# Performance work log

Measured on AMD Instinct MI355X. Metric: run time of the kernel, lower is better.

The kernel has to match this reference:

```python
import jax, jax.numpy as jnp
import numpy as np

NUM_HEADS = 4  # nn.MultiheadAttention(num_heads=4)


def setup_inputs() -> dict:
    key = jax.random.key(0)
    ks = jax.random.split(key, 9)
    E, D, B, S = 16, 128, 8, 512
    H2 = D // 2
    s = 0.05
    return {
        "lstm_features": jax.random.normal(ks[0], (B, S, D), dtype=jnp.float32),
        "Wqkv": jax.random.normal(ks[1], (E, 3 * D, D), dtype=jnp.float32) * s,
        "bqkv": jax.random.normal(ks[2], (E, 3 * D), dtype=jnp.float32) * s,
        "Wo": jax.random.normal(ks[3], (E, D, D), dtype=jnp.float32) * s,
        "bo": jax.random.normal(ks[4], (E, D), dtype=jnp.float32) * s,
        "W1": jax.random.normal(ks[5], (E, H2, D), dtype=jnp.float32) * s,
        "b1": jax.random.normal(ks[6], (E, H2), dtype=jnp.float32) * s,
        "W2": jax.random.normal(ks[7], (E, 1, H2), dtype=jnp.float32) * s,
        "b2": jax.random.normal(ks[8], (E, 1), dtype=jnp.float32) * s,
    }


def reference(lstm_features, Wqkv, bqkv, Wo, bo, W1, b1, W2, b2):
    # lstm_features: [B, S, D]; params stacked over E=num_events.
    B, S, D = lstm_features.shape
    E = Wqkv.shape[0]
    H = NUM_HEADS
    Dh = D // H

    # Grouped in-projection for all events at once: [E, B, S, 3D]
    qkv = jnp.einsum("bsd,ekd->ebsk", lstm_features, Wqkv) + bqkv[:, None, None, :]
    q, k, v = jnp.split(qkv, 3, axis=-1)  # each [E, B, S, D]

    def heads(t):  # [E,B,S,D] -> [E,B,H,S,Dh]
        return t.reshape(E, B, S, H, Dh).transpose(0, 1, 3, 2, 4)

    q, k, v = heads(q), heads(k), heads(v)

    scale = 1.0 / jnp.sqrt(jnp.asarray(Dh, dtype=lstm_features.dtype))
    scores = jnp.einsum("ebhqd,ebhkd->ebhqk", q, k) * scale  # [E,B,H,S,S]
    attn = jax.nn.softmax(scores, axis=-1)
    ctx = jnp.einsum("ebhqk,ebhkd->ebhqd", attn, v)  # [E,B,H,S,Dh]
    ctx = ctx.transpose(0, 1, 3, 2, 4).reshape(E, B, S, D)

    attended = jnp.einsum("ebsd,eod->ebso", ctx, Wo) + bo[:, None, None, :]

    # Per-event MLP head: D -> D//2 -> 1 (dropout is identity in eval)
    h = jax.nn.relu(jnp.einsum("ebsd,ehd->ebsh", attended, W1) + b1[:, None, None, :])
    logits = jnp.einsum("ebsh,eoh->ebso", h, W2) + b2[:, None, None, :]  # [E,B,S,1]
    logits = logits[..., 0]  # [E,B,S]

    # torch.stack(..., dim=2) -> [B, S, E]
    return logits.transpose(1, 2, 0)
```

## Files before the change

### kernel.cpp

```cpp
#include <hip/hip_runtime.h>
#include <hip/hip_bf16.h>


#define E_ 16
#define B_ 8
#define S_ 512
#define D_ 128
#define H_ 4
#define DH_ 32
#define H2_ 64
#define M_ (B_ * S_)
#define QK_SCALE_L2E 0.25503472437616588f

typedef __attribute__((ext_vector_type(4))) short bf16x4;
typedef __attribute__((ext_vector_type(8))) short bf16x8;
typedef __attribute__((ext_vector_type(4))) float f32x4;

__device__ __forceinline__ short f2bf(float f) {
    unsigned u = __builtin_bit_cast(unsigned, f);
    u += 0x7fffu + ((u >> 16) & 1u);
    return (short)(u >> 16);
}

__device__ __forceinline__ unsigned pk2(float lo, float hi) {
    __hip_bfloat162 t = __float22bfloat162_rn(make_float2(lo, hi));
    unsigned r;
    __builtin_memcpy(&r, &t, sizeof(r));
    return r;
}

__device__ __forceinline__ bf16x8 cat8(bf16x4 lo, bf16x4 hi) {
    return __builtin_shufflevector(lo, hi, 0, 1, 2, 3, 4, 5, 6, 7);
}

__global__ __launch_bounds__(256) void convert_kernel(
    const float* __restrict__ x, const float* __restrict__ w,
    const float* __restrict__ wo, const float* __restrict__ w1,
    short* __restrict__ xbf, short* __restrict__ wbf,
    short* __restrict__ wobf, short* __restrict__ w1bf)
{
    const int XN  = (M_ * D_) / 8;
    const int WN  = (E_ * 3 * D_ * D_) / 8;
    const int WON = (E_ * D_ * D_) / 8;
    const int W1N = (E_ * H2_ * D_) / 8;
    int idx = blockIdx.x * 256 + threadIdx.x;
    const float* src; short* dst; int off;
    if (idx < XN)                        { src = x;  dst = xbf;  off = idx; }
    else if (idx < XN + WN)              { src = w;  dst = wbf;  off = idx - XN; }
    else if (idx < XN + WN + WON)        { src = wo; dst = wobf; off = idx - XN - WN; }
    else if (idx < XN + WN + WON + W1N)  { src = w1; dst = w1bf; off = idx - XN - WN - WON; }
    else return;
    float4 v0 = *(const float4*)&src[(size_t)off * 8];
    float4 v1 = *(const float4*)&src[(size_t)off * 8 + 4];
    bf16x8 o;
    o[0] = f2bf(v0.x); o[1] = f2bf(v0.y); o[2] = f2bf(v0.z); o[3] = f2bf(v0.w);
    o[4] = f2bf(v1.x); o[5] = f2bf(v1.y); o[6] = f2bf(v1.z); o[7] = f2bf(v1.w);
    *(bf16x8*)&dst[(size_t)off * 8] = o;
}

__global__ __launch_bounds__(256) void qkv_mfma_kernel(
    const short* __restrict__ xbf,
    const short* __restrict__ wbf,
    const float* __restrict__ bqkv,
    short* __restrict__ q, short* __restrict__ k, short* __restrict__ v)
{
    __shared__ __align__(16) char lds[2 * 64 * 136 * 2];
    short (*xs)[136] = (short(*)[136])lds;
    short (*ws)[136] = (short(*)[136])(lds + 64 * 136 * 2);

    const int ct = blockIdx.x;
    const int rt = blockIdx.y;
    const int e  = blockIdx.z;
    const int tid = threadIdx.x;
    const int w    = tid >> 6;
    const int lane = tid & 63;
    const int l15  = lane & 15;
    const int g    = lane >> 4;

    #pragma unroll
    for (int p = 0; p < 4; ++p) {
        int idx = tid + p * 256;
        int row = idx >> 4, c8 = (idx & 15) * 8;
        *(bf16x8*)&xs[row][c8] =
            *(const bf16x8*)&xbf[(size_t)(rt * 64 + row) * 128 + c8];
        *(bf16x8*)&ws[row][c8] =
            *(const bf16x8*)&wbf[((size_t)e * 384 + ct * 64 + row) * 128 + c8];
    }
    __syncthreads();

    const int n0 = (w & 1) * 32;
    const int m0 = (w >> 1) * 32;
    f32x4 acc00 = {0.f,0.f,0.f,0.f}, acc01 = {0.f,0.f,0.f,0.f};
    f32x4 acc10 = {0.f,0.f,0.f,0.f}, acc11 = {0.f,0.f,0.f,0.f};

    #pragma unroll
    for (int kk = 0; kk < 128; kk += 32) {
        bf16x8 A0 = cat8(*(const bf16x4*)&ws[n0      + l15][kk + 4 * g],
                         *(const bf16x4*)&ws[n0      + l15][kk + 16 + 4 * g]);
        bf16x8 A1 = cat8(*(const bf16x4*)&ws[n0 + 16 + l15][kk + 4 * g],
                         *(const bf16x4*)&ws[n0 + 16 + l15][kk + 16 + 4 * g]);
        bf16x8 B0 = cat8(*(const bf16x4*)&xs[m0      + l15][kk + 4 * g],
                         *(const bf16x4*)&xs[m0      + l15][kk + 16 + 4 * g]);
        bf16x8 B1 = cat8(*(const bf16x4*)&xs[m0 + 16 + l15][kk + 4 * g],
                         *(const bf16x4*)&xs[m0 + 16 + l15][kk + 16 + 4 * g]);
        acc00 = __builtin_amdgcn_mfma_f32_16x16x32_bf16(A0, B0, acc00, 0, 0, 0);
        acc01 = __builtin_amdgcn_mfma_f32_16x16x32_bf16(A0, B1, acc01, 0, 0, 0);
        acc10 = __builtin_amdgcn_mfma_f32_16x16x32_bf16(A1, B0, acc10, 0, 0, 0);
        acc11 = __builtin_amdgcn_mfma_f32_16x16x32_bf16(A1, B1, acc11, 0, 0, 0);
    }

    if (ct < 4) {
        short* dst = (ct < 2) ? q : k;
        const float scale = (ct < 2) ? QK_SCALE_L2E : 1.0f;
        #define STORE_QK(ACC, NS, MS) {                                          \
            const int jb = ct * 64 + n0 + (NS) * 16 + 4 * g;                     \
            const int d  = jb & 127;                                             \
            const int h  = d >> 5, dh = d & 31;                                  \
            const float b0 = bqkv[e * 384 + jb + 0];                             \
            const float b1 = bqkv[e * 384 + jb + 1];                             \
            const float b2 = bqkv[e * 384 + jb + 2];                             \
            const float b3 = bqkv[e * 384 + jb + 3];                             \
            const int m  = rt * 64 + m0 + (MS) * 16 + l15;                       \
            const int bb = m >> 9, s = m & 511;                                  \
            bf16x4 o;                                                            \
            o[0] = f2bf((ACC[0] + b0) * scale);                                  \
            o[1] = f2bf((ACC[1] + b1) * scale);                                  \
            o[2] = f2bf((ACC[2] + b2) * scale);                                  \
            o[3] = f2bf((ACC[3] + b3) * scale);                                  \
            *(bf16x4*)&dst[((((size_t)e * B_ + bb) * H_ + h) * S_ + s) * DH_ + dh] = o; \
        }
        STORE_QK(acc00, 0, 0); STORE_QK(acc01, 0, 1);
        STORE_QK(acc10, 1, 0); STORE_QK(acc11, 1, 1);
        #undef STORE_QK
    } else {
        __syncthreads();
        float (*rp)[68] = (float(*)[68])lds;
        #define RP(ACC, NS, MS) {                                                \
            const int jl = n0 + (NS) * 16 + 4 * g;                               \
            const int ml = m0 + (MS) * 16 + l15;                                 \
            rp[jl + 0][ml] = ACC[0]; rp[jl + 1][ml] = ACC[1];                    \
            rp[jl + 2][ml] = ACC[2]; rp[jl + 3][ml] = ACC[3];                    \
        }
        RP(acc00, 0, 0); RP(acc01, 0, 1); RP(acc10, 1, 0); RP(acc11, 1, 1);
        #undef RP
        __syncthreads();
        const int bb = (rt * 64) >> 9;
        const int sb = (rt * 64) & 511;
        #pragma unroll
        for (int p = 0; p < 2; ++p) {
            int task = tid + p * 256;
            int jl = task >> 3, sc = (task & 7) * 8;
            const int col = ct * 64 + jl;
            const int d = col & 127, h = d >> 5, dh = d & 31;
            const float bias = bqkv[e * 384 + col];
            bf16x8 o;
            #pragma unroll
            for (int j = 0; j < 8; ++j) o[j] = f2bf(rp[jl][sc + j] + bias);
            *(bf16x8*)&v[((((size_t)e * B_ + bb) * H_ + h) * DH_ + dh) * S_ + sb + sc] = o;
        }
    }
}

__global__ __launch_bounds__(512) void attn_kernel(
    const short* __restrict__ q, const short* __restrict__ k,
    const short* __restrict__ vt, short* __restrict__ ctxbf)
{
    __shared__ alignas(16) short Ks[128][40];
    __shared__ alignas(16) short VTs[32][520];

    const int qh  = blockIdx.x;
    const int bh  = blockIdx.y;
    const int e   = blockIdx.z;
    const int tid = threadIdx.x;
    const int w    = tid >> 6;
    const int lane = tid & 63;
    const int l15  = lane & 15;
    const int g    = lane >> 4;

    const size_t base = ((size_t)e * 32 + bh) * (S_ * DH_);
    const short* qg = q  + base;
    const short* kg = k  + base;
    const short* vg = vt + base;

    {
        int d = tid >> 4, c0 = (tid & 15) * 32;
        const uint4* src = (const uint4*)(vg + (size_t)d * S_ + c0);
        uint4* dst = (uint4*)((char*)&VTs[0][0] + (size_t)d * 1040 + c0 * 2);
        dst[0] = src[0]; dst[1] = src[1]; dst[2] = src[2]; dst[3] = src[3];
    }
    {
        int row = tid >> 2, ch = (tid & 3) * 8;
        *(uint4*)((char*)&Ks[0][0] + (size_t)row * 80 + ch * 2) =
            *(const uint4*)(kg + (size_t)row * DH_ + ch);
    }
    bf16x8 bq[2];
    #pragma unroll
    for (int qf = 0; qf < 2; ++qf) {
        const short* qp = qg + (size_t)(qh * 256 + w * 32 + qf * 16 + l15) * DH_;
        bq[qf] = cat8(*(const bf16x4*)(qp + 4 * g),
                      *(const bf16x4*)(qp + 16 + 4 * g));
    }
    __syncthreads();

    f32x4 acc0[2] = {}, acc1[2] = {};
    float lsum[2] = {0.f, 0.f};

    for (int quarter = 0; quarter < 4; ++quarter) {
        for (int kt = 0; kt < 4; ++kt) {
            bf16x8 ka[2];
            #pragma unroll
            for (int tt = 0; tt < 2; ++tt) {
                const int row_l = (kt * 2 + tt) * 16 + l15;
                const char* kp = (const char*)&Ks[0][0] + (size_t)row_l * 80 + g * 8;
                ka[tt] = cat8(*(const bf16x4*)kp, *(const bf16x4*)(kp + 32));
            }
            const int keyb = quarter * 128 + kt * 32;
            const char* vp = (const char*)&VTs[0][0] + (size_t)l15 * 1040 + (keyb + 4 * g) * 2;
            bf16x8 va0 = cat8(*(const bf16x4*)vp, *(const bf16x4*)(vp + 32));
            const char* vp1 = vp + 16 * 1040;
            bf16x8 va1 = cat8(*(const bf16x4*)vp1, *(const bf16x4*)(vp1 + 32));

            #pragma unroll
            for (int qf = 0; qf < 2; ++qf) {
                f32x4 z = {0.f, 0.f, 0.f, 0.f};
                f32x4 s0 = __builtin_amdgcn_mfma_f32_16x16x32_bf16(ka[0], bq[qf], z, 0, 0, 0);
                f32x4 s1 = __builtin_amdgcn_mfma_f32_16x16x32_bf16(ka[1], bq[qf], z, 0, 0, 0);
                float p0 = __builtin_amdgcn_exp2f(s0[0]);
                float p1 = __builtin_amdgcn_exp2f(s0[1]);
                float p2 = __builtin_amdgcn_exp2f(s0[2]);
                float p3 = __builtin_amdgcn_exp2f(s0[3]);
                float p4 = __builtin_amdgcn_exp2f(s1[0]);
                float p5 = __builtin_amdgcn_exp2f(s1[1]);
                float p6 = __builtin_amdgcn_exp2f(s1[2]);
                float p7 = __builtin_amdgcn_exp2f(s1[3]);
                lsum[qf] += ((p0 + p1) + (p2 + p3)) + ((p4 + p5) + (p6 + p7));
                uint4 uu = make_uint4(pk2(p0, p1), pk2(p2, p3),
                                      pk2(p4, p5), pk2(p6, p7));
                bf16x8 pf = __builtin_bit_cast(bf16x8, uu);
                acc0[qf] = __builtin_amdgcn_mfma_f32_16x16x32_bf16(va0, pf, acc0[qf], 0, 0, 0);
                acc1[qf] = __builtin_amdgcn_mfma_f32_16x16x32_bf16(va1, pf, acc1[qf], 0, 0, 0);
            }
        }
        if (quarter < 3) {
            __syncthreads();
            int row = tid >> 2, ch = (tid & 3) * 8;
            *(uint4*)((char*)&Ks[0][0] + (size_t)row * 80 + ch * 2) =
                *(const uint4*)(kg + (size_t)((quarter + 1) * 128 + row) * DH_ + ch);
            __syncthreads();
        }
    }

    const int b = bh >> 2, h = bh & 3;
    #pragma unroll
    for (int qf = 0; qf < 2; ++qf) {
        float ls = lsum[qf];
        ls += __shfl_xor(ls, 16);
        ls += __shfl_xor(ls, 32);
        const float inv = 1.0f / ls;
        const int qrow = qh * 256 + w * 32 + qf * 16 + l15;
        short* cg = ctxbf + (((size_t)(e * B_ + b) * S_ + qrow) * D_ + h * DH_);
        bf16x4 o0, o1;
        #pragma unroll
        for (int r = 0; r < 4; ++r) {
            o0[r] = f2bf(acc0[qf][r] * inv);
            o1[r] = f2bf(acc1[qf][r] * inv);
        }
        *(bf16x4*)&cg[4 * g]      = o0;
        *(bf16x4*)&cg[16 + 4 * g] = o1;
    }
}

__global__ __launch_bounds__(256) void head_mfma_kernel(
    const short* __restrict__ ctxbf,
    const short* __restrict__ wobf,
    const float* __restrict__ bo,
    const short* __restrict__ w1bf,
    const float* __restrict__ b1,
    const float* __restrict__ W2,
    const float* __restrict__ b2,
    float* __restrict__ out)
{
    __shared__ alignas(16) short Wos[128][136];
    __shared__ alignas(16) short cts[64][136];

    const int mt  = blockIdx.x;
    const int e   = blockIdx.y;
    const int tid = threadIdx.x;
    const int w    = tid >> 6;
    const int lane = tid & 63;
    const int l15  = lane & 15;
    const int g    = lane >> 4;

    #pragma unroll
    for (int p = 0; p < 8; ++p) {
        int idx = tid + p * 256;
        int row = idx >> 4, c8 = (idx & 15) * 8;
        *(bf16x8*)&Wos[row][c8] =
            *(const bf16x8*)&wobf[((size_t)e * 128 + row) * 128 + c8];
    }
    #pragma unroll
    for (int p = 0; p < 4; ++p) {
        int idx = tid + p * 256;
        int row = idx >> 4, c8 = (idx & 15) * 8;
        *(bf16x8*)&cts[row][c8] =
            *(const bf16x8*)&ctxbf[((size_t)e * M_ + mt * 64 + row) * 128 + c8];
    }
    __syncthreads();

    f32x4 accA[8] = {};
    #pragma unroll
    for (int kk = 0; kk < 128; kk += 32) {
        bf16x8 a = cat8(*(const bf16x4*)&cts[w * 16 + l15][kk + 4 * g],
                        *(const bf16x4*)&cts[w * 16 + l15][kk + 16 + 4 * g]);
        #pragma unroll
        for (int t = 0; t < 8; ++t) {
            bf16x8 bfr = cat8(*(const bf16x4*)&Wos[t * 16 + l15][kk + 4 * g],
                              *(const bf16x4*)&Wos[t * 16 + l15][kk + 16 + 4 * g]);
            accA[t] = __builtin_amdgcn_mfma_f32_16x16x32_bf16(a, bfr, accA[t], 0, 0, 0);
        }
    }
    __syncthreads();

    #pragma unroll
    for (int p = 0; p < 4; ++p) {
        int idx = tid + p * 256;
        int row = idx >> 4, c8 = (idx & 15) * 8;
        *(bf16x8*)&Wos[row][c8] =
            *(const bf16x8*)&w1bf[((size_t)e * 64 + row) * 128 + c8];
    }
    #pragma unroll
    for (int t = 0; t < 8; ++t) {
        const float bov = bo[e * 128 + t * 16 + l15];
        #pragma unroll
        for (int r = 0; r < 4; ++r)
            cts[w * 16 + 4 * g + r][t * 16 + l15] = f2bf(accA[t][r] + bov);
    }
    __syncthreads();

    f32x4 accB[4] = {};
    #pragma unroll
    for (int kk = 0; kk < 128; kk += 32) {
        bf16x8 a = cat8(*(const bf16x4*)&cts[w * 16 + l15][kk + 4 * g],
                        *(const bf16x4*)&cts[w * 16 + l15][kk + 16 + 4 * g]);
        #pragma unroll
        for (int t = 0; t < 4; ++t) {
            bf16x8 bfr = cat8(*(const bf16x4*)&Wos[t * 16 + l15][kk + 4 * g],
                              *(const bf16x4*)&Wos[t * 16 + l15][kk + 16 + 4 * g]);
            accB[t] = __builtin_amdgcn_mfma_f32_16x16x32_bf16(a, bfr, accB[t], 0, 0, 0);
        }
    }

    float b1v[4], w2v[4];
    #pragma unroll
    for (int t = 0; t < 4; ++t) {
        b1v[t] = b1[e * 64 + t * 16 + l15];
        w2v[t] = W2[e * 64 + t * 16 + l15];
    }
    const float b2v = b2[e];
    #pragma unroll
    for (int r = 0; r < 4; ++r) {
        float s = 0.f;
        #pragma unroll
        for (int t = 0; t < 4; ++t)
            s += fmaxf(accB[t][r] + b1v[t], 0.f) * w2v[t];
        s += __shfl_xor(s, 1);
        s += __shfl_xor(s, 2);
        s += __shfl_xor(s, 4);
        s += __shfl_xor(s, 8);
        if (l15 == 0) {
            const int m = mt * 64 + w * 16 + 4 * g + r;
            const int bb = m >> 9, ss = m & 511;
            out[((size_t)(bb * S_ + ss)) * E_ + e] = s + b2v;
        }
    }
}

extern "C" void kernel_launch(void* const* d_in, const int* in_sizes, int n_in,
                              void* d_out, int out_size, void* d_ws, size_t ws_size,
                              hipStream_t stream) {
    const float* x    = (const float*)d_in[0];
    const float* Wqkv = (const float*)d_in[1];
    const float* bqkv = (const float*)d_in[2];
    const float* Wo   = (const float*)d_in[3];
    const float* bo   = (const float*)d_in[4];
    const float* W1   = (const float*)d_in[5];
    const float* b1   = (const float*)d_in[6];
    const float* W2   = (const float*)d_in[7];
    const float* b2   = (const float*)d_in[8];
    float* out = (float*)d_out;

    const size_t SZ = (size_t)E_ * B_ * H_ * S_ * DH_;
    short* qb    = (short*)d_ws;
    short* kb    = qb + SZ;
    short* vtb   = kb + SZ;
    short* ctxbf = vtb + SZ;
    short* xbf   = ctxbf + SZ;
    short* wbf   = xbf + (size_t)M_ * D_;
    short* wobf  = wbf + (size_t)E_ * 3 * D_ * D_;
    short* w1bf  = wobf + (size_t)E_ * D_ * D_;

    convert_kernel<<<dim3(832), 256, 0, stream>>>(x, Wqkv, Wo, W1, xbf, wbf, wobf, w1bf);
    qkv_mfma_kernel<<<dim3(6, 64, 16), 256, 0, stream>>>(xbf, wbf, bqkv, qb, kb, vtb);
    attn_kernel<<<dim3(2, 32, 16), 512, 0, stream>>>(qb, kb, vtb, ctxbf);
    head_mfma_kernel<<<dim3(64, 16), 256, 0, stream>>>(ctxbf, wobf, bo, w1bf, b1, W2, b2, out);
}
```

Baseline: 77.48 us.

## Stage all keys in LDS once and read V fragments directly from global

The attention kernel now loads all 512 keys of the head into LDS in a single pass, which removes the per-quarter reloads and the barriers inside the key loop. V^T is no longer staged in LDS; each wave reads its V fragments straight from global memory (through L1/L2) every iteration. The goal is to remove the synchronisation and staging overhead, but it adds many small uncoalesced 8-byte global loads in the inner loop and a latency risk on the PV MFMA path.

```diff
diff --git a/kernel.cpp b/kernel.cpp
--- a/kernel.cpp
+++ b/kernel.cpp
@@ -165,8 +165,7 @@
     const short* __restrict__ q, const short* __restrict__ k,
     const short* __restrict__ vt, short* __restrict__ ctxbf)
 {
-    __shared__ alignas(16) short Ks[128][40];
-    __shared__ alignas(16) short VTs[32][520];
+    __shared__ alignas(16) short Ks[512][40];
 
     const int qh  = blockIdx.x;
     const int bh  = blockIdx.y;
@@ -183,15 +182,9 @@
     const short* vg = vt + base;
 
     {
-        int d = tid >> 4, c0 = (tid & 15) * 32;
-        const uint4* src = (const uint4*)(vg + (size_t)d * S_ + c0);
-        uint4* dst = (uint4*)((char*)&VTs[0][0] + (size_t)d * 1040 + c0 * 2);
+        const uint4* src = (const uint4*)(kg + (size_t)tid * DH_);
+        uint4* dst = (uint4*)((char*)&Ks[0][0] + (size_t)tid * 80);
         dst[0] = src[0]; dst[1] = src[1]; dst[2] = src[2]; dst[3] = src[3];
-    }
-    {
-        int row = tid >> 2, ch = (tid & 3) * 8;
-        *(uint4*)((char*)&Ks[0][0] + (size_t)row * 80 + ch * 2) =
-            *(const uint4*)(kg + (size_t)row * DH_ + ch);
     }
     bf16x8 bq[2];
     #pragma unroll
@@ -205,48 +198,40 @@
     f32x4 acc0[2] = {}, acc1[2] = {};
     float lsum[2] = {0.f, 0.f};
 
-    for (int quarter = 0; quarter < 4; ++quarter) {
-        for (int kt = 0; kt < 4; ++kt) {
-            bf16x8 ka[2];
-            #pragma unroll
-            for (int tt = 0; tt < 2; ++tt) {
-                const int row_l = (kt * 2 + tt) * 16 + l15;
-                const char* kp = (const char*)&Ks[0][0] + (size_t)row_l * 80 + g * 8;
-                ka[tt] = cat8(*(const bf16x4*)kp, *(const bf16x4*)(kp + 32));
-            }
-            const int keyb = quarter * 128 + kt * 32;
-            const char* vp = (const char*)&VTs[0][0] + (size_t)l15 * 1040 + (keyb + 4 * g) * 2;
-            bf16x8 va0 = cat8(*(const bf16x4*)vp, *(const bf16x4*)(vp + 32));
-            const char* vp1 = vp + 16 * 1040;
-            bf16x8 va1 = cat8(*(const bf16x4*)vp1, *(const bf16x4*)(vp1 + 32));
-
-            #pragma unroll
-            for (int qf = 0; qf < 2; ++qf) {
-                f32x4 z = {0.f, 0.f, 0.f, 0.f};
-                f32x4 s0 = __builtin_amdgcn_mfma_f32_16x16x32_bf16(ka[0], bq[qf], z, 0, 0, 0);
-                f32x4 s1 = __builtin_amdgcn_mfma_f32_16x16x32_bf16(ka[1], bq[qf], z, 0, 0, 0);
-                float p0 = __builtin_amdgcn_exp2f(s0[0]);
-                float p1 = __builtin_amdgcn_exp2f(s0[1]);
-                float p2 = __builtin_amdgcn_exp2f(s0[2]);
-                float p3 = __builtin_amdgcn_exp2f(s0[3]);
-                float p4 = __builtin_amdgcn_exp2f(s1[0]);
-                float p5 = __builtin_amdgcn_exp2f(s1[1]);
-                float p6 = __builtin_amdgcn_exp2f(s1[2]);
-                float p7 = __builtin_amdgcn_exp2f(s1[3]);
-                lsum[qf] += ((p0 + p1) + (p2 + p3)) + ((p4 + p5) + (p6 + p7));
-                uint4 uu = make_uint4(pk2(p0, p1), pk2(p2, p3),
-                                      pk2(p4, p5), pk2(p6, p7));
-                bf16x8 pf = __builtin_bit_cast(bf16x8, uu);
-                acc0[qf] = __builtin_amdgcn_mfma_f32_16x16x32_bf16(va0, pf, acc0[qf], 0, 0, 0);
-                acc1[qf] = __builtin_amdgcn_mfma_f32_16x16x32_bf16(va1, pf, acc1[qf], 0, 0, 0);
-            }
-        }
-        if (quarter < 3) {
-            __syncthreads();
-            int row = tid >> 2, ch = (tid & 3) * 8;
-            *(uint4*)((char*)&Ks[0][0] + (size_t)row * 80 + ch * 2) =
-                *(const uint4*)(kg + (size_t)((quarter + 1) * 128 + row) * DH_ + ch);
-            __syncthreads();
+    #pragma unroll 2
+    for (int kt = 0; kt < 16; ++kt) {
+        bf16x8 ka[2];
+        #pragma unroll
+        for (int tt = 0; tt < 2; ++tt) {
+            const int row_l = (kt * 2 + tt) * 16 + l15;
+            const char* kp = (const char*)&Ks[0][0] + (size_t)row_l * 80 + g * 8;
+            ka[tt] = cat8(*(const bf16x4*)kp, *(const bf16x4*)(kp + 32));
+        }
+        const int keyb = kt * 32;
+        const short* vgp = vg + (size_t)l15 * S_ + keyb + 4 * g;
+        bf16x8 va0 = cat8(*(const bf16x4*)vgp, *(const bf16x4*)(vgp + 16));
+        const short* vgp1 = vgp + 16 * S_;
+        bf16x8 va1 = cat8(*(const bf16x4*)vgp1, *(const bf16x4*)(vgp1 + 16));
+
+        #pragma unroll
+        for (int qf = 0; qf < 2; ++qf) {
+            f32x4 z = {0.f, 0.f, 0.f, 0.f};
+            f32x4 s0 = __builtin_amdgcn_mfma_f32_16x16x32_bf16(ka[0], bq[qf], z, 0, 0, 0);
+            f32x4 s1 = __builtin_amdgcn_mfma_f32_16x16x32_bf16(ka[1], bq[qf], z, 0, 0, 0);
+            float p0 = __builtin_amdgcn_exp2f(s0[0]);
+            float p1 = __builtin_amdgcn_exp2f(s0[1]);
+            float p2 = __builtin_amdgcn_exp2f(s0[2]);
+            float p3 = __builtin_amdgcn_exp2f(s0[3]);
+            float p4 = __builtin_amdgcn_exp2f(s1[0]);
+            float p5 = __builtin_amdgcn_exp2f(s1[1]);
+            float p6 = __builtin_amdgcn_exp2f(s1[2]);
+            float p7 = __builtin_amdgcn_exp2f(s1[3]);
+            lsum[qf] += ((p0 + p1) + (p2 + p3)) + ((p4 + p5) + (p6 + p7));
+            uint4 uu = make_uint4(pk2(p0, p1), pk2(p2, p3),
+                                  pk2(p4, p5), pk2(p6, p7));
+            bf16x8 pf = __builtin_bit_cast(bf16x8, uu);
+            acc0[qf] = __builtin_amdgcn_mfma_f32_16x16x32_bf16(va0, pf, acc0[qf], 0, 0, 0);
+            acc1[qf] = __builtin_amdgcn_mfma_f32_16x16x32_bf16(va1, pf, acc1[qf], 0, 0, 0);
         }
     }
 
```

Measured after the change: 106.4 us. +37.4%, slower.
